# Kernel tuning notes

Measured on AMD Instinct MI355X. Metric: run time of the kernel, lower is better.

## Reference

```python
import jax, jax.numpy as jnp
import numpy as np

NUM_LAYERS = 12
D = 256          # d_model
H = 8            # n_head
DK = D // H      # qk_dim = v_dim = 32
FFD = 1024       # ffd_dim
B, L = 32, 448
EPS = 1e-6
MAXLEN = 500


def _sinusoidal_pos_emb(maxlen, hidden_dim):
    depth = hidden_dim / 2
    positions = np.arange(maxlen, dtype=np.float32)[:, None]
    depths = np.arange(depth, dtype=np.float32)[None, :] / depth
    angle_rads = positions * (1.0 / np.power(10000.0, depths))
    pe = np.concatenate([np.sin(angle_rads), np.cos(angle_rads)], axis=-1)
    return jnp.asarray(pe, jnp.float32)


def setup_inputs() -> dict:
    key = jax.random.key(0)
    ks = jax.random.split(key, 16)
    s = 0.02
    inp = {
        "x": jax.random.normal(ks[0], (B, L, D), jnp.float32),
        "mask": jnp.zeros((B, L), jnp.bool_),
        "pos_emb": _sinusoidal_pos_emb(MAXLEN - 1, D)[:L],  # [L, D]
        "Wq": jax.random.normal(ks[1], (NUM_LAYERS, D, D), jnp.float32) * s,
        "bq": jnp.zeros((NUM_LAYERS, D), jnp.float32),
        "Wk": jax.random.normal(ks[2], (NUM_LAYERS, D, D), jnp.float32) * s,
        "bk": jnp.zeros((NUM_LAYERS, D), jnp.float32),
        "Wv": jax.random.normal(ks[3], (NUM_LAYERS, D, D), jnp.float32) * s,
        "bv": jnp.zeros((NUM_LAYERS, D), jnp.float32),
        "Wo": jax.random.normal(ks[4], (NUM_LAYERS, D, D), jnp.float32) * s,
        "bo": jnp.zeros((NUM_LAYERS, D), jnp.float32),
        "W1": jax.random.normal(ks[5], (NUM_LAYERS, D, FFD), jnp.float32) * s,
        "bf1": jnp.zeros((NUM_LAYERS, FFD), jnp.float32),
        "W2": jax.random.normal(ks[6], (NUM_LAYERS, FFD, D), jnp.float32) * s,
        "bf2": jnp.zeros((NUM_LAYERS, D), jnp.float32),
        "ln1_g": jnp.ones((NUM_LAYERS, D), jnp.float32),
        "ln1_b": jnp.zeros((NUM_LAYERS, D), jnp.float32),
        "ln2_g": jnp.ones((NUM_LAYERS, D), jnp.float32),
        "ln2_b": jnp.zeros((NUM_LAYERS, D), jnp.float32),
    }
    return inp


def _layer_norm(x, g, b):
    mu = jnp.mean(x, axis=-1, keepdims=True)
    var = jnp.mean(jnp.square(x - mu), axis=-1, keepdims=True)
    return (x - mu) * jax.lax.rsqrt(var + EPS) * g + b


def _encoder_forward(x, mask, pos_emb, Wq, bq, Wk, bk, Wv, bv, Wo, bo,
                     W1, bf1, W2, bf2, ln1_g, ln1_b, ln2_g, ln2_b):
    Bx, Lx, _ = x.shape
    scale = 1.0 / np.sqrt(DK)
    x = x + pos_emb[None, :Lx, :]
    mask_b = mask[:, None, None, :]  # [B,1,1,L], True = masked
    for i in range(NUM_LAYERS):
        # --- pre-norm attention ---
        nx = _layer_norm(x, ln1_g[i], ln1_b[i])
        q = (nx @ Wq[i] + bq[i]).reshape(Bx, Lx, H, DK)
        k = (nx @ Wk[i] + bk[i]).reshape(Bx, Lx, H, DK)
        v = (nx @ Wv[i] + bv[i]).reshape(Bx, Lx, H, DK)
        dot = jnp.einsum("bihd,bjhd->bhij", q, k) * scale
        dot = jnp.where(mask_b, -10000.0, dot)
        attn = jax.nn.softmax(dot, axis=-1)
        o = jnp.einsum("bhij,bjhd->bihd", attn, v).reshape(Bx, Lx, D)
        x = x + (o @ Wo[i] + bo[i])
        # --- pre-norm FFN (exact GELU, as torch nn.GELU) ---
        nx2 = _layer_norm(x, ln2_g[i], ln2_b[i])
        h = jax.nn.gelu(nx2 @ W1[i] + bf1[i], approximate=False)
        x = x + (h @ W2[i] + bf2[i])
    return x


def reference(x, mask, pos_emb, Wq, bq, Wk, bk, Wv, bv, Wo, bo,
              W1, bf1, W2, bf2, ln1_g, ln1_b, ln2_g, ln2_b):
    return _encoder_forward(x, mask, pos_emb, Wq, bq, Wk, bk, Wv, bv, Wo, bo,
                            W1, bf1, W2, bf2, ln1_g, ln1_b, ln2_g, ln2_b)
```

## Files before the change

kernel.cpp:

```cpp
#include <hip/hip_runtime.h>

#define NL 12
#define DM 256
#define FFDIM 1024
#define BBATCH 32
#define LSEQ 448
#define MTOK (BBATCH*LSEQ)
#define EPSF 1e-6f
#define QSCALE 0.17677669529663687f

typedef __attribute__((ext_vector_type(8))) short bf16x8;
typedef __attribute__((ext_vector_type(4))) float f32x4;
typedef unsigned short u16;
typedef unsigned int u32;

__device__ __forceinline__ u16 f2bf(float f) {
    union { float f; u32 u; } v; v.f = f;
    u32 r = v.u + 0x7fffu + ((v.u >> 16) & 1u);
    return (u16)(r >> 16);
}
__device__ __forceinline__ float gelu_exact(float x) {
    return 0.5f * x * (1.0f + erff(x * 0.70710678118654752f));
}
__device__ __forceinline__ void gload16(const u16* g, u16* l) {
    __builtin_amdgcn_global_load_lds(
        (const __attribute__((address_space(1))) u32*)g,
        (__attribute__((address_space(3))) u32*)l, 16, 0, 0);
}

__global__ __launch_bounds__(256) void add_pos_k(
    const float* __restrict__ x, const float* __restrict__ pe, float* __restrict__ out)
{
    int i = blockIdx.x * 256 + threadIdx.x;
    float4 xv = ((const float4*)x)[i];
    float4 pv = ((const float4*)pe)[i % (LSEQ * DM / 4)];
    float4 r;
    r.x = xv.x + pv.x; r.y = xv.y + pv.y; r.z = xv.z + pv.z; r.w = xv.w + pv.w;
    ((float4*)out)[i] = r;
}

__global__ __launch_bounds__(256) void ln_k(
    const float* __restrict__ x, const float* __restrict__ g,
    const float* __restrict__ b, u16* __restrict__ out)
{
    const int w = threadIdx.x >> 6, lane = threadIdx.x & 63;
    const int row = blockIdx.x * 4 + w;
    float4 v = ((const float4*)(x + (size_t)row * DM))[lane];
    float s = v.x + v.y + v.z + v.w;
#pragma unroll
    for (int off = 32; off; off >>= 1) s += __shfl_xor(s, off);
    float mu = s * (1.0f / 256.0f);
    float d0 = v.x - mu, d1 = v.y - mu, d2 = v.z - mu, d3 = v.w - mu;
    float sq = d0*d0 + d1*d1 + d2*d2 + d3*d3;
#pragma unroll
    for (int off = 32; off; off >>= 1) sq += __shfl_xor(sq, off);
    float rs = rsqrtf(sq * (1.0f / 256.0f) + EPSF);
    float4 gv = ((const float4*)g)[lane];
    float4 bv = ((const float4*)b)[lane];
    ushort4 o;
    o.x = f2bf(d0 * rs * gv.x + bv.x);
    o.y = f2bf(d1 * rs * gv.y + bv.y);
    o.z = f2bf(d2 * rs * gv.z + bv.z);
    o.w = f2bf(d3 * rs * gv.w + bv.w);
    *(ushort4*)(out + (size_t)row * DM + lane * 4) = o;
}

__global__ __launch_bounds__(256) void twt_k(
    const float* __restrict__ in, u16* __restrict__ out,
    int K, int N, int in_lstride, int out_lstride)
{
    __shared__ float tl[32][33];
    const int l = blockIdx.z;
    const int n0 = blockIdx.x * 32, k0 = blockIdx.y * 32;
    const int tx = threadIdx.x & 31, ty = threadIdx.x >> 5;
    const float* src = in + (size_t)l * in_lstride;
#pragma unroll
    for (int i = 0; i < 4; ++i)
        tl[ty + 8*i][tx] = src[(size_t)(k0 + ty + 8*i) * N + n0 + tx];
    __syncthreads();
    u16* dst = out + (size_t)l * out_lstride;
#pragma unroll
    for (int i = 0; i < 4; ++i)
        dst[(size_t)(n0 + ty + 8*i) * K + k0 + tx] = f2bf(tl[tx][ty + 8*i]);
}

__global__ __launch_bounds__(256) void pack_bias_k(
    const float* __restrict__ bq, const float* __restrict__ bk,
    const float* __restrict__ bv, float* __restrict__ bqkv)
{
    int i = blockIdx.x * 256 + threadIdx.x;
    if (i >= NL * 768) return;
    int l = i / 768, c = i % 768;
    float v = (c < 256) ? bq[l*256 + c] : (c < 512) ? bk[l*256 + c - 256] : bv[l*256 + c - 512];
    bqkv[i] = v;
}

__global__ __launch_bounds__(256) void vt_k(
    const u16* __restrict__ qkv, u16* __restrict__ vtg)
{
    __shared__ u16 tl[32][33];
    const int kt = blockIdx.x, h = blockIdx.y, b = blockIdx.z;
    const int tx = threadIdx.x & 31, ty = threadIdx.x >> 5;
#pragma unroll
    for (int i = 0; i < 4; ++i)
        tl[ty + 8*i][tx] = qkv[(size_t)(b*LSEQ + kt*32 + ty + 8*i) * 768 + 512 + h*32 + tx];
    __syncthreads();
#pragma unroll
    for (int i = 0; i < 4; ++i)
        vtg[((size_t)(b*8 + h)*32 + ty + 8*i) * 448 + kt*32 + tx] = tl[tx][ty + 8*i];
}

template<int BM, int BN, int EPI>
__global__ __launch_bounds__(256, (BM == 64) ? 4 : 3) void mm_k(
    const u16* __restrict__ A, int lda, const u16* __restrict__ Bt,
    const float* __restrict__ bias, void* __restrict__ C, int ldc, int K)
{
    __shared__ u16 As[2 * BM * 32];
    __shared__ u16 Bs[2 * BN * 32];
    constexpr int MT = (BM == 128) ? 4 : 1;
    constexpr int APANEL = BM * 32;
    constexpr int BPANEL = BN * 32;
    const int tid = threadIdx.x;
    const int by = blockIdx.x, bx = blockIdx.y;
    const int w = tid >> 6, lane = tid & 63;
    const int lm = lane & 15, lk = lane >> 4;
    const int m0 = (BM == 128) ? ((w >> 1) * 64) : (w * 16);
    const int n0 = (BM == 128) ? ((w & 1) * 64) : 0;
    const int lrow = lane >> 2, lcol = (lane & 3) * 8;

    const u16* Ab = A + (size_t)(by * BM) * lda;
    const u16* Bb = Bt + (size_t)(bx * BN) * K;

    f32x4 zz = {0.f, 0.f, 0.f, 0.f};
    f32x4 acc[MT][4];
#pragma unroll
    for (int i = 0; i < MT; ++i)
#pragma unroll
        for (int j = 0; j < 4; ++j) acc[i][j] = zz;

    for (int k0 = 0; k0 < K; k0 += 64) {
        __syncthreads();
#pragma unroll
        for (int p = 0; p < 2; ++p) {
            if constexpr (BM == 128) {
#pragma unroll
                for (int i = 0; i < 2; ++i) {
                    int seg = w * 2 + i;
                    gload16(Ab + (size_t)(seg * 16 + lrow) * lda + k0 + p * 32 + lcol,
                            &As[p * APANEL + seg * 512]);
                    gload16(Bb + (size_t)(seg * 16 + lrow) * K + k0 + p * 32 + lcol,
                            &Bs[p * BPANEL + seg * 512]);
                }
            } else {
                gload16(Ab + (size_t)(w * 16 + lrow) * lda + k0 + p * 32 + lcol,
                        &As[p * APANEL + w * 512]);
                gload16(Bb + (size_t)(w * 16 + lrow) * K + k0 + p * 32 + lcol,
                        &Bs[p * BPANEL + w * 512]);
            }
        }
        __syncthreads();

#pragma unroll
        for (int p = 0; p < 2; ++p) {
            bf16x8 af[MT], bfr[4];
#pragma unroll
            for (int mt = 0; mt < MT; ++mt)
                af[mt] = *(const bf16x8*)&As[p * APANEL + (m0 + mt*16 + lm)*32 + lk*8];
#pragma unroll
            for (int nt = 0; nt < 4; ++nt)
                bfr[nt] = *(const bf16x8*)&Bs[p * BPANEL + (n0 + nt*16 + lm)*32 + lk*8];
#pragma unroll
            for (int mt = 0; mt < MT; ++mt)
#pragma unroll
                for (int nt = 0; nt < 4; ++nt)
                    acc[mt][nt] = __builtin_amdgcn_mfma_f32_16x16x32_bf16(af[mt], bfr[nt], acc[mt][nt], 0, 0, 0);
        }
    }

    float bv[4];
#pragma unroll
    for (int nt = 0; nt < 4; ++nt) bv[nt] = bias[bx*BN + n0 + nt*16 + lm];
#pragma unroll
    for (int mt = 0; mt < MT; ++mt) {
#pragma unroll
        for (int r = 0; r < 4; ++r) {
            int grow = by*BM + m0 + mt*16 + lk*4 + r;
#pragma unroll
            for (int nt = 0; nt < 4; ++nt) {
                int gcol = bx*BN + n0 + nt*16 + lm;
                float vv = acc[mt][nt][r] + bv[nt];
                if constexpr (EPI == 0) {
                    ((u16*)C)[(size_t)grow * ldc + gcol] = f2bf(vv);
                } else if constexpr (EPI == 1) {
                    ((u16*)C)[(size_t)grow * ldc + gcol] = f2bf(gelu_exact(vv));
                } else if constexpr (EPI == 3) {
                    float qs = (gcol < 256) ? QSCALE : 1.0f;
                    ((u16*)C)[(size_t)grow * ldc + gcol] = f2bf(vv * qs);
                } else {
                    float* p = (float*)C + (size_t)grow * ldc + gcol;
                    *p += vv;
                }
            }
        }
    }
}

__global__ __launch_bounds__(256, 4) void attn_k(
    const u16* __restrict__ qkv, const u16* __restrict__ vtg,
    const unsigned char* __restrict__ mask, u16* __restrict__ ob)
{
    __shared__ u16 Klds[448 * 32];
    __shared__ u16 Plds[4][16 * 68];
    const int tid = threadIdx.x, w = tid >> 6, lane = tid & 63;
    const int lm = lane & 15, lk = lane >> 4;
    const int bid = blockIdx.x;
    const int bh = bid & 255, sg = bid >> 8;
    const int b = bh >> 3, h = bh & 7;
    const size_t rowbase = (size_t)b * LSEQ;

#pragma unroll
    for (int i = 0; i < 7; ++i) {
        int seg = w * 7 + i;
        gload16(qkv + (rowbase + seg * 16 + (lane >> 2)) * 768 + 256 + h * 32 + (lane & 3) * 8,
                &Klds[seg * 512]);
    }
    unsigned mbits = 0;
#pragma unroll
    for (int t = 0; t < 28; ++t)
        mbits |= (mask[b * LSEQ + t * 16 + lm] ? 1u : 0u) << t;
    __syncthreads();

    const u16* Vb = vtg + (size_t)bh * 32 * 448;
    f32x4 zz = {0.f, 0.f, 0.f, 0.f};

    const int q0 = (sg * 4 + w) * 16;
    bf16x8 qf = *(const bf16x8*)(qkv + (rowbase + q0 + lm) * 768 + h * 32 + lk * 8);

    float mx[4] = {-1e30f, -1e30f, -1e30f, -1e30f};
#pragma unroll
    for (int t = 0; t < 28; ++t) {
        bf16x8 kf = *(const bf16x8*)&Klds[(t*16 + lm)*32 + lk*8];
        f32x4 s = __builtin_amdgcn_mfma_f32_16x16x32_bf16(qf, kf, zz, 0, 0, 0);
        bool m = (mbits >> t) & 1;
#pragma unroll
        for (int r = 0; r < 4; ++r) {
            float v = m ? -10000.0f : s[r];
            mx[r] = fmaxf(mx[r], v);
        }
    }
#pragma unroll
    for (int off = 1; off < 16; off <<= 1)
#pragma unroll
        for (int r = 0; r < 4; ++r) mx[r] = fmaxf(mx[r], __shfl_xor(mx[r], off));

    f32x4 oacc[2] = {zz, zz};
    float sum[4] = {0.f, 0.f, 0.f, 0.f};
    u16* P = &Plds[w][0];
#pragma unroll
    for (int cc = 0; cc < 7; ++cc) {
#pragma unroll
        for (int tt = 0; tt < 4; ++tt) {
            int t = cc*4 + tt;
            bf16x8 kf = *(const bf16x8*)&Klds[(t*16 + lm)*32 + lk*8];
            f32x4 s = __builtin_amdgcn_mfma_f32_16x16x32_bf16(qf, kf, zz, 0, 0, 0);
            bool m = (mbits >> t) & 1;
#pragma unroll
            for (int r = 0; r < 4; ++r) {
                float v = m ? -10000.0f : s[r];
                float e = __expf(v - mx[r]);
                sum[r] += e;
                P[(lk*4 + r)*68 + tt*16 + lm] = f2bf(e);
            }
        }
        bf16x8 pa0 = *(const bf16x8*)&P[lm*68 + lk*8];
        bf16x8 pa1 = *(const bf16x8*)&P[lm*68 + 32 + lk*8];
#pragma unroll
        for (int dt = 0; dt < 2; ++dt) {
            bf16x8 vb0 = *(const bf16x8*)(Vb + (size_t)(dt*16 + lm)*448 + cc*64 + lk*8);
            bf16x8 vb1 = *(const bf16x8*)(Vb + (size_t)(dt*16 + lm)*448 + cc*64 + 32 + lk*8);
            oacc[dt] = __builtin_amdgcn_mfma_f32_16x16x32_bf16(pa0, vb0, oacc[dt], 0, 0, 0);
            oacc[dt] = __builtin_amdgcn_mfma_f32_16x16x32_bf16(pa1, vb1, oacc[dt], 0, 0, 0);
        }
    }
#pragma unroll
    for (int off = 1; off < 16; off <<= 1)
#pragma unroll
        for (int r = 0; r < 4; ++r) sum[r] += __shfl_xor(sum[r], off);
    float inv[4];
#pragma unroll
    for (int r = 0; r < 4; ++r) inv[r] = 1.0f / sum[r];

#pragma unroll
    for (int dt = 0; dt < 2; ++dt)
#pragma unroll
        for (int r = 0; r < 4; ++r)
            ob[(rowbase + q0 + lk*4 + r)*256 + h*32 + dt*16 + lm] = f2bf(oacc[dt][r] * inv[r]);
}

extern "C" void kernel_launch(void* const* d_in, const int* in_sizes, int n_in,
                              void* d_out, int out_size, void* d_ws, size_t ws_size,
                              hipStream_t stream)
{
    const float* x_in = (const float*)d_in[0];
    const unsigned char* mask = (const unsigned char*)d_in[1];
    const float* pe   = (const float*)d_in[2];
    const float* Wq = (const float*)d_in[3];
    const float* bq = (const float*)d_in[4];
    const float* Wk = (const float*)d_in[5];
    const float* bk = (const float*)d_in[6];
    const float* Wv = (const float*)d_in[7];
    const float* bv = (const float*)d_in[8];
    const float* Wo = (const float*)d_in[9];
    const float* bo = (const float*)d_in[10];
    const float* W1 = (const float*)d_in[11];
    const float* bf1 = (const float*)d_in[12];
    const float* W2 = (const float*)d_in[13];
    const float* bf2 = (const float*)d_in[14];
    const float* ln1_g = (const float*)d_in[15];
    const float* ln1_b = (const float*)d_in[16];
    const float* ln2_g = (const float*)d_in[17];
    const float* ln2_b = (const float*)d_in[18];

    float* x = (float*)d_out;
    u16* ws = (u16*)d_ws;
    u16* nx   = ws;
    u16* qkv  = nx + 3670016;
    u16* ob   = qkv + 11010048;
    u16* vtg  = ob + 3670016;
    u16* hb   = qkv;
    u16* wqkvt = vtg + 3670016;
    u16* wot  = wqkvt + 2359296;
    u16* w1t  = wot + 786432;
    u16* w2t  = w1t + 3145728;
    float* bqkv = (float*)(w2t + 3145728);

    add_pos_k<<<MTOK * DM / 1024, 256, 0, stream>>>(x_in, pe, x);

    twt_k<<<dim3(8, 8, NL), 256, 0, stream>>>(Wq, wqkvt,          256, 256, 65536, 196608);
    twt_k<<<dim3(8, 8, NL), 256, 0, stream>>>(Wk, wqkvt + 65536,  256, 256, 65536, 196608);
    twt_k<<<dim3(8, 8, NL), 256, 0, stream>>>(Wv, wqkvt + 131072, 256, 256, 65536, 196608);
    twt_k<<<dim3(8, 8, NL), 256, 0, stream>>>(Wo, wot, 256, 256, 65536, 65536);
    twt_k<<<dim3(32, 8, NL), 256, 0, stream>>>(W1, w1t, 256, 1024, 262144, 262144);
    twt_k<<<dim3(8, 32, NL), 256, 0, stream>>>(W2, w2t, 1024, 256, 262144, 262144);
    pack_bias_k<<<(NL * 768 + 255) / 256, 256, 0, stream>>>(bq, bk, bv, bqkv);

    for (int l = 0; l < NL; ++l) {
        ln_k<<<MTOK / 4, 256, 0, stream>>>(x, ln1_g + l*256, ln1_b + l*256, nx);
        mm_k<128, 128, 3><<<dim3(112, 6), 256, 0, stream>>>(
            nx, 256, wqkvt + (size_t)l*196608, bqkv + l*768, qkv, 768, 256);
        vt_k<<<dim3(14, 8, 32), 256, 0, stream>>>(qkv, vtg);
        attn_k<<<1792, 256, 0, stream>>>(qkv, vtg, mask, ob);
        mm_k<64, 64, 2><<<dim3(224, 4), 256, 0, stream>>>(
            ob, 256, wot + (size_t)l*65536, bo + l*256, x, 256, 256);
        ln_k<<<MTOK / 4, 256, 0, stream>>>(x, ln2_g + l*256, ln2_b + l*256, nx);
        mm_k<128, 128, 1><<<dim3(112, 8), 256, 0, stream>>>(
            nx, 256, w1t + (size_t)l*262144, bf1 + l*1024, hb, 1024, 256);
        mm_k<64, 64, 2><<<dim3(224, 4), 256, 0, stream>>>(
            hb, 1024, w2t + (size_t)l*262144, bf2 + l*256, x, 256, 1024);
    }
}
```

Measured before the change: 1.456 ms.

## Fuse V transpose into QKV epilogue, drop softmax max pass, retile output GEMMs

The QKV GEMM epilogue now writes V directly in transposed per-head layout, which removes the separate vt_k kernel and its extra read and write of V. Q is pre-scaled by scale*log2(e), and attention drops the first QK^T pass that only found the row max. It now computes exp2 of the raw scores and zeroes masked keys, halving the QK MFMA work. The Wo and W2 GEMMs switch to 128x64 tiles to halve the grid. Dropping max subtraction risks overflow for large scores and gives NaN for fully masked rows, and the V-transpose stores are strided scatters.

```diff
diff --git a/kernel.cpp b/kernel.cpp
--- a/kernel.cpp
+++ b/kernel.cpp
@@ -7,7 +7,7 @@
 #define LSEQ 448
 #define MTOK (BBATCH*LSEQ)
 #define EPSF 1e-6f
-#define QSCALE 0.17677669529663687f
+#define QSCALE_LOG2E (0.17677669529663687f * 1.4426950408889634f)
 
 typedef __attribute__((ext_vector_type(8))) short bf16x8;
 typedef __attribute__((ext_vector_type(4))) float f32x4;
@@ -95,37 +95,23 @@
     bqkv[i] = v;
 }
 
-__global__ __launch_bounds__(256) void vt_k(
-    const u16* __restrict__ qkv, u16* __restrict__ vtg)
-{
-    __shared__ u16 tl[32][33];
-    const int kt = blockIdx.x, h = blockIdx.y, b = blockIdx.z;
-    const int tx = threadIdx.x & 31, ty = threadIdx.x >> 5;
-#pragma unroll
-    for (int i = 0; i < 4; ++i)
-        tl[ty + 8*i][tx] = qkv[(size_t)(b*LSEQ + kt*32 + ty + 8*i) * 768 + 512 + h*32 + tx];
-    __syncthreads();
-#pragma unroll
-    for (int i = 0; i < 4; ++i)
-        vtg[((size_t)(b*8 + h)*32 + ty + 8*i) * 448 + kt*32 + tx] = tl[tx][ty + 8*i];
-}
-
 template<int BM, int BN, int EPI>
-__global__ __launch_bounds__(256, (BM == 64) ? 4 : 3) void mm_k(
+__global__ __launch_bounds__(256, (BN == 64) ? 4 : 3) void mm_k(
     const u16* __restrict__ A, int lda, const u16* __restrict__ Bt,
-    const float* __restrict__ bias, void* __restrict__ C, int ldc, int K)
+    const float* __restrict__ bias, void* __restrict__ C, int ldc, int K,
+    u16* __restrict__ vtg)
 {
     __shared__ u16 As[2 * BM * 32];
     __shared__ u16 Bs[2 * BN * 32];
-    constexpr int MT = (BM == 128) ? 4 : 1;
+    constexpr int MT = (BM * BN) / 4096;
     constexpr int APANEL = BM * 32;
     constexpr int BPANEL = BN * 32;
     const int tid = threadIdx.x;
     const int by = blockIdx.x, bx = blockIdx.y;
     const int w = tid >> 6, lane = tid & 63;
     const int lm = lane & 15, lk = lane >> 4;
-    const int m0 = (BM == 128) ? ((w >> 1) * 64) : (w * 16);
-    const int n0 = (BM == 128) ? ((w & 1) * 64) : 0;
+    const int m0 = (BN == 128) ? ((w >> 1) * 64) : (w * (MT * 16));
+    const int n0 = (BN == 128) ? ((w & 1) * 64) : 0;
     const int lrow = lane >> 2, lcol = (lane & 3) * 8;
 
     const u16* Ab = A + (size_t)(by * BM) * lda;
@@ -148,12 +134,19 @@
                     int seg = w * 2 + i;
                     gload16(Ab + (size_t)(seg * 16 + lrow) * lda + k0 + p * 32 + lcol,
                             &As[p * APANEL + seg * 512]);
+                }
+            } else {
+                gload16(Ab + (size_t)(w * 16 + lrow) * lda + k0 + p * 32 + lcol,
+                        &As[p * APANEL + w * 512]);
+            }
+            if constexpr (BN == 128) {
+#pragma unroll
+                for (int i = 0; i < 2; ++i) {
+                    int seg = w * 2 + i;
                     gload16(Bb + (size_t)(seg * 16 + lrow) * K + k0 + p * 32 + lcol,
                             &Bs[p * BPANEL + seg * 512]);
                 }
             } else {
-                gload16(Ab + (size_t)(w * 16 + lrow) * lda + k0 + p * 32 + lcol,
-                        &As[p * APANEL + w * 512]);
                 gload16(Bb + (size_t)(w * 16 + lrow) * K + k0 + p * 32 + lcol,
                         &Bs[p * BPANEL + w * 512]);
             }
@@ -185,6 +178,11 @@
 #pragma unroll
         for (int r = 0; r < 4; ++r) {
             int grow = by*BM + m0 + mt*16 + lk*4 + r;
+            u32 bidx = 0; int srow = 0;
+            if constexpr (EPI == 3) {
+                bidx = (u32)grow / 448u;
+                srow = grow - (int)bidx * 448;
+            }
 #pragma unroll
             for (int nt = 0; nt < 4; ++nt) {
                 int gcol = bx*BN + n0 + nt*16 + lm;
@@ -194,8 +192,15 @@
                 } else if constexpr (EPI == 1) {
                     ((u16*)C)[(size_t)grow * ldc + gcol] = f2bf(gelu_exact(vv));
                 } else if constexpr (EPI == 3) {
-                    float qs = (gcol < 256) ? QSCALE : 1.0f;
-                    ((u16*)C)[(size_t)grow * ldc + gcol] = f2bf(vv * qs);
+                    if (gcol < 256) {
+                        ((u16*)C)[(size_t)grow * ldc + gcol] = f2bf(vv * QSCALE_LOG2E);
+                    } else if (gcol < 512) {
+                        ((u16*)C)[(size_t)grow * ldc + gcol] = f2bf(vv);
+                    } else {
+                        int c = gcol - 512;
+                        int h = c >> 5, d = c & 31;
+                        vtg[((size_t)(bidx*8 + h)*32 + d)*448 + srow] = f2bf(vv);
+                    }
                 } else {
                     float* p = (float*)C + (size_t)grow * ldc + gcol;
                     *p += vv;
@@ -236,23 +241,6 @@
     const int q0 = (sg * 4 + w) * 16;
     bf16x8 qf = *(const bf16x8*)(qkv + (rowbase + q0 + lm) * 768 + h * 32 + lk * 8);
 
-    float mx[4] = {-1e30f, -1e30f, -1e30f, -1e30f};
-#pragma unroll
-    for (int t = 0; t < 28; ++t) {
-        bf16x8 kf = *(const bf16x8*)&Klds[(t*16 + lm)*32 + lk*8];
-        f32x4 s = __builtin_amdgcn_mfma_f32_16x16x32_bf16(qf, kf, zz, 0, 0, 0);
-        bool m = (mbits >> t) & 1;
-#pragma unroll
-        for (int r = 0; r < 4; ++r) {
-            float v = m ? -10000.0f : s[r];
-            mx[r] = fmaxf(mx[r], v);
-        }
-    }
-#pragma unroll
-    for (int off = 1; off < 16; off <<= 1)
-#pragma unroll
-        for (int r = 0; r < 4; ++r) mx[r] = fmaxf(mx[r], __shfl_xor(mx[r], off));
-
     f32x4 oacc[2] = {zz, zz};
     float sum[4] = {0.f, 0.f, 0.f, 0.f};
     u16* P = &Plds[w][0];
@@ -266,8 +254,7 @@
             bool m = (mbits >> t) & 1;
 #pragma unroll
             for (int r = 0; r < 4; ++r) {
-                float v = m ? -10000.0f : s[r];
-                float e = __expf(v - mx[r]);
+                float e = m ? 0.f : exp2f(s[r]);
                 sum[r] += e;
                 P[(lk*4 + r)*68 + tt*16 + lm] = f2bf(e);
             }
@@ -347,15 +334,14 @@
     for (int l = 0; l < NL; ++l) {
         ln_k<<<MTOK / 4, 256, 0, stream>>>(x, ln1_g + l*256, ln1_b + l*256, nx);
         mm_k<128, 128, 3><<<dim3(112, 6), 256, 0, stream>>>(
-            nx, 256, wqkvt + (size_t)l*196608, bqkv + l*768, qkv, 768, 256);
-        vt_k<<<dim3(14, 8, 32), 256, 0, stream>>>(qkv, vtg);
+            nx, 256, wqkvt + (size_t)l*196608, bqkv + l*768, qkv, 768, 256, vtg);
         attn_k<<<1792, 256, 0, stream>>>(qkv, vtg, mask, ob);
-        mm_k<64, 64, 2><<<dim3(224, 4), 256, 0, stream>>>(
-            ob, 256, wot + (size_t)l*65536, bo + l*256, x, 256, 256);
+        mm_k<128, 64, 2><<<dim3(112, 4), 256, 0, stream>>>(
+            ob, 256, wot + (size_t)l*65536, bo + l*256, x, 256, 256, nullptr);
         ln_k<<<MTOK / 4, 256, 0, stream>>>(x, ln2_g + l*256, ln2_b + l*256, nx);
         mm_k<128, 128, 1><<<dim3(112, 8), 256, 0, stream>>>(
-            nx, 256, w1t + (size_t)l*262144, bf1 + l*1024, hb, 1024, 256);
-        mm_k<64, 64, 2><<<dim3(224, 4), 256, 0, stream>>>(
-            hb, 1024, w2t + (size_t)l*262144, bf2 + l*256, x, 256, 1024);
-    }
-}
+            nx, 256, w1t + (size_t)l*262144, bf1 + l*1024, hb, 1024, 256, nullptr);
+        mm_k<128, 64, 2><<<dim3(112, 4), 256, 0, stream>>>(
+            hb, 1024, w2t + (size_t)l*262144, bf2 + l*256, x, 256, 1024, nullptr);
+    }
+}
```

After: 1.473 ms. No clear change (+1.2%).
